# Performance work log

Hardware: AMD Instinct MI355X
Metric: run time of the kernel (lower is better)

Reference implementation:

```python
import jax, jax.numpy as jnp
import numpy as np
import math
from math import factorial

EPS = 1e-8
N_ATOMS = 20000
K_NEI = 32
N_RBF = 12
RBF_GAMMA = 1.0
DIMS = [(3, 24), (24, 12), (12, 4)]
# (i, f, o) = (input angular order, filter order, output order), from Convolution.C
CG_PATHS = [(0,0,0),(0,1,1),(1,0,1),(1,1,0),(1,1,1),(1,1,2),(0,2,2),(1,2,1),(1,2,2),(2,2,0),(2,2,1),(2,2,2),(2,0,2),(2,1,1),(2,1,2)]


def _su2_cg(j1, m1, j2, m2, j3, m3):
    if m3 != m1 + m2:
        return 0.0
    f = factorial
    vmin = int(max(-j1 + j2 + m3, -j1 + m1, 0))
    vmax = int(min(j2 + j3 + m1, j3 - j1 + j2, j3 + m3))
    c = ((2 * j3 + 1) * f(j3 + j1 - j2) * f(j3 - j1 + j2) * f(j1 + j2 - j3)
         * f(j3 + m3) * f(j3 - m3)
         / (f(j1 + j2 + j3 + 1) * f(j1 - m1) * f(j1 + m1) * f(j2 - m2) * f(j2 + m2))) ** 0.5
    s = 0.0
    for v in range(vmin, vmax + 1):
        s += (-1) ** (v + j2 + m2) * f(j2 + j3 + m1 - v) * f(j1 - m1 + v) / (
            f(v) * f(j3 - j1 + j2 - v) * f(j3 + m3 - v) * f(j1 - j2 - m3 + v))
    return c * s


def _q(l):
    # change of basis real->complex spherical harmonics (e3nn convention)
    q = np.zeros((2 * l + 1, 2 * l + 1), dtype=complex)
    for m in range(-l, 0):
        q[l + m, l + abs(m)] = 1 / np.sqrt(2)
        q[l + m, l - abs(m)] = -1j / np.sqrt(2)
    q[l, l] = 1.0
    for m in range(1, l + 1):
        q[l + m, l + abs(m)] = (-1) ** m / np.sqrt(2)
        q[l + m, l - abs(m)] = 1j * (-1) ** m / np.sqrt(2)
    return (-1j) ** l * q


def _real_cg(i, f, o):
    C = np.zeros((2 * i + 1, 2 * f + 1, 2 * o + 1), dtype=complex)
    for a, m1 in enumerate(range(-i, i + 1)):
        for b, m2 in enumerate(range(-f, f + 1)):
            for c, m3 in enumerate(range(-o, o + 1)):
                C[a, b, c] = _su2_cg(i, m1, f, m2, o, m3)
    C = np.einsum('ij,kl,mn,ikn->jlm', _q(i), _q(f), np.conj(_q(o).T), C)
    return np.real(C).transpose(2, 0, 1).astype(np.float32)  # [2o+1, 2i+1, 2f+1]


CG = {(i, f, o): jnp.asarray(_real_cg(i, f, o)) for (i, f, o) in CG_PATHS}
RBF_MU = jnp.asarray(np.linspace(0.0, 8.0, N_RBF).astype(np.float32))


def _sh(vec):
    # real spherical harmonics as in class Y (l=1 is the raw vector, l=2 divided by r^2)
    x, y, z = vec[..., 0], vec[..., 1], vec[..., 2]
    r2 = jnp.maximum(x * x + y * y + z * z, EPS)
    y2 = jnp.stack([x * y / r2,
                    y * z / r2,
                    (-x * x - y * y + 2.0 * z * z) / (2.0 * math.sqrt(3.0) * r2),
                    z * x / r2,
                    (x * x - y * y) / (2.0 * r2)], axis=-1)
    return {0: jnp.ones(vec.shape[:-1] + (1,), vec.dtype), 1: vec, 2: y2}


def _ssp(x):  # eta: shifted softplus (SchNet-style scalar nonlinearity)
    return jax.nn.softplus(x) - math.log(2.0)


def _self_interaction(V, w, b):
    O = {k: jnp.einsum('ncm,dc->ndm', Vk, w) for k, Vk in V.items()}
    O[0] = O[0] + b[None, :, None]  # bias only on angular order 0
    return O


def _model(V, nei_idx, Ys, rbf, siA_w, siA_b, rw1, rb1, rw2, rb2, siB_w, siB_b, nl_b):
    V = _self_interaction(V, siA_w, siA_b)
    N, C = nei_idx.shape[0], rw2.shape[1]
    O = {l: jnp.zeros((N, C, 2 * l + 1), rbf.dtype) for l in range(3)}
    for p, (i, f, o) in enumerate(CG_PATHS):
        # per-path radial MLP: 12 -> 12 (relu) -> C
        h = jax.nn.relu(jnp.einsum('nkb,hb->nkh', rbf, rw1[p]) + rb1[p])
        r = jnp.einsum('nkh,ch->nkc', h, rw2[p]) + rb2[p]              # [N,K,C]
        Vg = V[i][nei_idx]                                              # [N,K,C,2i+1]
        cif = jnp.einsum('nkc,nkf,nkci->ncif', r, Ys[f], Vg)            # sum over neighbors
        O[o] = O[o] + jnp.einsum('oif,ncif->nco', CG[(i, f, o)], cif)
    # Norm: per-atom L2 norm over (channel, m)
    V = {k: Vk / jnp.sqrt(jnp.maximum(jnp.sum(Vk * Vk, axis=(1, 2), keepdims=True), EPS))
         for k, Vk in O.items()}
    V = _self_interaction(V, siB_w, siB_b)
    # NonLinearity (faithful to source: norm is taken over ALL atoms and m, per channel)
    out = {0: _ssp(V[0])}
    for k in (1, 2):
        temp = jnp.sqrt(jnp.einsum('acm,acm->c', V[k], V[k])) + nl_b[k - 1]
        out[k] = V[k] * temp[None, :, None]
    return out


def _forward(atom_types, nei_idx, nei_vec, layers, dense):
    N = atom_types.shape[0]
    dt = nei_vec.dtype
    V = {0: jax.nn.one_hot(atom_types, 3, dtype=dt)[:, :, None],
         1: jnp.zeros((N, 3, 3), dt),
         2: jnp.zeros((N, 3, 5), dt)}
    dist = jnp.sqrt(jnp.maximum(jnp.sum(nei_vec * nei_vec, axis=-1), EPS))   # [N,K]
    rbf = jnp.exp(-RBF_GAMMA * (dist[..., None] - RBF_MU) ** 2)              # [N,K,12]
    Ys = _sh(nei_vec)
    for lp in layers:
        V = _model(V, nei_idx, Ys, rbf, *lp)
    E = jnp.sum(V[0], axis=0)[:, 0]                                          # [4]
    dw1, db1, dw2, db2, dw3, db3 = dense
    E = jax.nn.elu(dw1 @ E + db1)
    E = dw2 @ E + db2
    E = dw3 @ E + db3
    return E  # [1]


def setup_inputs() -> dict:
    key = jax.random.key(0)
    ks = iter(jax.random.split(key, 64))
    inp = {}
    inp['atom_types'] = jax.random.randint(next(ks), (N_ATOMS,), 0, 3, dtype=jnp.int32)
    inp['nei_idx'] = jax.random.randint(next(ks), (N_ATOMS, K_NEI), 0, N_ATOMS, dtype=jnp.int32)
    inp['nei_vec'] = jax.random.normal(next(ks), (N_ATOMS, K_NEI, 3), jnp.float32) * 2.0
    for l, (din, dout) in enumerate(DIMS, start=1):
        inp[f'l{l}_siA_w'] = jax.random.normal(next(ks), (dout, din)) / np.sqrt(din)
        inp[f'l{l}_siA_b'] = jnp.zeros((dout,))
        inp[f'l{l}_rw1'] = jax.random.normal(next(ks), (15, N_RBF, N_RBF)) / np.sqrt(N_RBF)
        inp[f'l{l}_rb1'] = jnp.zeros((15, N_RBF))
        inp[f'l{l}_rw2'] = jax.random.normal(next(ks), (15, dout, N_RBF)) / np.sqrt(N_RBF)
        inp[f'l{l}_rb2'] = jnp.zeros((15, dout))
        inp[f'l{l}_siB_w'] = jax.random.normal(next(ks), (dout, dout)) / np.sqrt(dout)
        inp[f'l{l}_siB_b'] = jnp.zeros((dout,))
        inp[f'l{l}_nl_b'] = jnp.zeros((2, dout))
    inp['dense_w1'] = jax.random.normal(next(ks), (4, 4)) * 0.5
    inp['dense_b1'] = jnp.zeros((4,))
    inp['dense_w2'] = jax.random.normal(next(ks), (256, 4)) * 0.5
    inp['dense_b2'] = jnp.zeros((256,))
    inp['dense_w3'] = jax.random.normal(next(ks), (1, 256)) / 16.0
    inp['dense_b3'] = jnp.zeros((1,))
    return inp


def reference(atom_types, nei_idx, nei_vec,
              l1_siA_w, l1_siA_b, l1_rw1, l1_rb1, l1_rw2, l1_rb2, l1_siB_w, l1_siB_b, l1_nl_b,
              l2_siA_w, l2_siA_b, l2_rw1, l2_rb1, l2_rw2, l2_rb2, l2_siB_w, l2_siB_b, l2_nl_b,
              l3_siA_w, l3_siA_b, l3_rw1, l3_rb1, l3_rw2, l3_rb2, l3_siB_w, l3_siB_b, l3_nl_b,
              dense_w1, dense_b1, dense_w2, dense_b2, dense_w3, dense_b3):
    layers = [
        (l1_siA_w, l1_siA_b, l1_rw1, l1_rb1, l1_rw2, l1_rb2, l1_siB_w, l1_siB_b, l1_nl_b),
        (l2_siA_w, l2_siA_b, l2_rw1, l2_rb1, l2_rw2, l2_rb2, l2_siB_w, l2_siB_b, l2_nl_b),
        (l3_siA_w, l3_siA_b, l3_rw1, l3_rb1, l3_rw2, l3_rb2, l3_siB_w, l3_siB_b, l3_nl_b),
    ]
    dense = (dense_w1, dense_b1, dense_w2, dense_b2, dense_w3, dense_b3)
    return _forward(atom_types, nei_idx, nei_vec, layers, dense)
```

## Files before the change

kernel.cpp:

```cpp
#include <hip/hip_runtime.h>
#include <math.h>

typedef long long i64;

#define EPSF 1e-8f

constexpr int NPATH = 15;
constexpr int PI_[NPATH] = {0,0,1,1,1,1,0,1,1,2,2,2,2,2,2};
constexpr int PF_[NPATH] = {0,1,0,1,1,1,2,2,2,2,2,2,0,1,1};
constexpr int PO_[NPATH] = {0,1,1,0,1,2,2,1,2,0,1,2,2,1,2};
constexpr int ISZ[NPATH] = {1,1,3,3,3,3,1,3,3,5,5,5,5,5,5};
constexpr int FSZ[NPATH] = {1,3,1,3,3,3,5,5,5,5,5,5,1,3,3};
constexpr int OSZ[NPATH] = {1,3,3,1,3,5,5,3,5,1,3,5,5,3,5};
constexpr int IBASE[NPATH] = {0,0,1,1,1,1,0,1,1,4,4,4,4,4,4};
constexpr int FBASE[NPATH] = {0,1,0,1,1,1,4,4,4,4,4,4,0,1,1};
constexpr int OBASE[NPATH] = {0,1,1,0,1,4,4,1,4,0,1,4,4,1,4};
constexpr int CGOFF[NPATH+1] = {0,1,10,19,28,55,100,125,170,245,270,345,470,495,540,615};
constexpr int GPOFF[NPATH+1] = {0,4,8,20,24,36,52,60,72,88,96,112,140,168,184,212};
constexpr int CGTOT = 615;
constexpr int GPTOT = 212;

__device__ double dfact(int n){ double r=1.0; for(int i=2;i<=n;++i) r*=(double)i; return r; }

__device__ double su2cg(int j1,int m1,int j2,int m2,int j3,int m3){
  if (m1+m2 != m3) return 0.0;
  int vmin = max(max(-j1+j2+m3, -j1+m1), 0);
  int vmax = min(min(j2+j3+m1, j3-j1+j2), j3+m3);
  if (vmax < vmin) return 0.0;
  double c = sqrt((double)(2*j3+1) * dfact(j3+j1-j2)*dfact(j3-j1+j2)*dfact(j1+j2-j3)
                  * dfact(j3+m3)*dfact(j3-m3)
                  / (dfact(j1+j2+j3+1)*dfact(j1-m1)*dfact(j1+m1)*dfact(j2-m2)*dfact(j2+m2)));
  double s = 0.0;
  for (int v=vmin; v<=vmax; ++v){
    double t = dfact(j2+j3+m1-v)*dfact(j1-m1+v)
             / (dfact(v)*dfact(j3-j1+j2-v)*dfact(j3+m3-v)*dfact(j1-j2-m3+v));
    s += ((v+j2+m2)&1) ? -t : t;
  }
  return c*s;
}

__device__ void qmat_lds(int l, double* qr, double* qi){
  for (int e=0;e<25;e++){ qr[e]=0.0; qi[e]=0.0; }
  const double s2 = 0.70710678118654752440;
  for (int m=-l; m<0; ++m){
    qr[(l+m)*5 + (l-m)] = s2;
    qi[(l+m)*5 + (l+m)] = -s2;
  }
  qr[l*5+l] = 1.0;
  for (int m=1; m<=l; ++m){
    double sg = (m&1)? -1.0 : 1.0;
    qr[(l+m)*5 + (l+m)] = sg*s2;
    qi[(l+m)*5 + (l-m)] = sg*s2;
  }
  if (l==1){
    for (int e=0;e<25;e++){ double r=qr[e], m=qi[e]; qr[e]=m; qi[e]=-r; }
  } else if (l==2){
    for (int e=0;e<25;e++){ qr[e]=-qr[e]; qi[e]=-qi[e]; }
  }
}

__global__ void cg_init_kernel(float* __restrict__ cg){
  int p = blockIdx.x;
  int li = PI_[p], lf = PF_[p], lo = PO_[p];
  int isz = 2*li+1, fsz = 2*lf+1, osz = 2*lo+1;
  __shared__ double sC[125];
  __shared__ double qir[25],qii[25],qfr[25],qfi[25],qor[25],qoi[25];
  if (threadIdx.x==0){
    qmat_lds(li,qir,qii); qmat_lds(lf,qfr,qfi); qmat_lds(lo,qor,qoi);
  }
  int tot = isz*fsz*osz;
  for (int e=threadIdx.x; e<tot; e+=blockDim.x){
    int a = e/(fsz*osz); int r = e%(fsz*osz); int b = r/osz; int n = r%osz;
    sC[e] = su2cg(li, a-li, lf, b-lf, lo, n-lo);
  }
  __syncthreads();
  for (int e=threadIdx.x; e<tot; e+=blockDim.x){
    int mo = e/(isz*fsz); int r = e%(isz*fsz); int ji = r/fsz; int lff = r%fsz;
    double acc = 0.0;
    for (int a=0;a<isz;a++) for(int b=0;b<fsz;b++) for(int n=0;n<osz;n++){
      double s = sC[(a*fsz+b)*osz+n];
      if (s==0.0) continue;
      double r1=qir[a*5+ji],  m1=qii[a*5+ji];
      double r2=qfr[b*5+lff], m2=qfi[b*5+lff];
      double r3=qor[n*5+mo],  m3=-qoi[n*5+mo];
      double rr = r1*r2 - m1*m2;
      double mm = r1*m2 + m1*r2;
      acc += (rr*r3 - mm*m3)*s;
    }
    cg[CGOFF[p] + (mo*isz+ji)*fsz + lff] = (float)acc;
  }
}

__device__ __forceinline__ float sspf(float x){
  float sp = (x > 20.f) ? x : log1pf(__expf(x));
  return sp - 0.69314718055994531f;
}

__global__ void siA1_kernel(const int* __restrict__ types, const float* __restrict__ w,
                            const float* __restrict__ b, float* __restrict__ Vp, int N){
  int idx = blockIdx.x*blockDim.x + threadIdx.x;
  if (idx >= N*24) return;
  int n = idx/24, d = idx%24;
  float v = w[d*3 + types[n]] + b[d];
  float* row = Vp + (i64)idx*12;
  row[0] = v;
  #pragma unroll
  for (int m=1;m<12;m++) row[m]=0.f;
}


template<int A, int P>
__device__ __forceinline__ void gphase(int t, const float* __restrict__ sY,
                                       const float* __restrict__ sCG, float* __restrict__ sG){
  if constexpr (P < NPATH){
    constexpr int gsz = OSZ[P]*ISZ[P];
    for (int e=t; e<gsz*A; e+=192){
      int a = e % A, rel = e / A;
      const float* cr = &sCG[CGOFF[P] + rel*FSZ[P]];
      const float* Yr = &sY[a*12 + FBASE[P]];
      float v = 0.f;
      #pragma unroll
      for (int f=0; f<FSZ[P]; ++f) v += cr[f]*Yr[f];
      sG[a*GPTOT + GPOFF[P] + rel] = v;
    }
    gphase<A,P+1>(t,sY,sCG,sG);
  }
}

template<int P, int V>
__device__ __forceinline__ void gstream(const float* __restrict__ sG_a,
                                        const float* vgr, float* acc){
  constexpr int gsz = OSZ[P]*ISZ[P];
  if constexpr (4*V < gsz){
    float4 g = *reinterpret_cast<const float4*>(&sG_a[GPOFF[P] + 4*V]);
    constexpr int e0 = 4*V;
    acc[OBASE[P] + (e0  )/ISZ[P]] += g.x * vgr[(e0  )%ISZ[P]];
    if constexpr (e0+1 < gsz) acc[OBASE[P] + (e0+1)/ISZ[P]] += g.y * vgr[(e0+1)%ISZ[P]];
    if constexpr (e0+2 < gsz) acc[OBASE[P] + (e0+2)/ISZ[P]] += g.z * vgr[(e0+2)%ISZ[P]];
    if constexpr (e0+3 < gsz) acc[OBASE[P] + (e0+3)/ISZ[P]] += g.w * vgr[(e0+3)%ISZ[P]];
    gstream<P,V+1>(sG_a,vgr,acc);
  }
}

template<int C, int P, int PEND>
__device__ __forceinline__ void ipath(const float* __restrict__ sw2c, const float* __restrict__ sb2,
                                      int c, const float* __restrict__ sh_a,
                                      const float* __restrict__ sG_a,
                                      const float* vg, float* acc){
  if constexpr (P < PEND){
    constexpr int NR2 = 15*C;
    float4 w0 = *reinterpret_cast<const float4*>(&sw2c[(0*NR2 + P*C + c)*4]);
    float4 w1 = *reinterpret_cast<const float4*>(&sw2c[(1*NR2 + P*C + c)*4]);
    float4 w2v= *reinterpret_cast<const float4*>(&sw2c[(2*NR2 + P*C + c)*4]);
    const float* h = &sh_a[P*12];
    float4 h0 = *reinterpret_cast<const float4*>(h);
    float4 h1 = *reinterpret_cast<const float4*>(h+4);
    float4 h2 = *reinterpret_cast<const float4*>(h+8);
    float rr = sb2[P*C+c]
      + w0.x*h0.x + w0.y*h0.y + w0.z*h0.z + w0.w*h0.w
      + w1.x*h1.x + w1.y*h1.y + w1.z*h1.z + w1.w*h1.w
      + w2v.x*h2.x + w2v.y*h2.y + w2v.z*h2.z + w2v.w*h2.w;
    float vgr[5];
    #pragma unroll
    for (int i=0; i<ISZ[P]; ++i) vgr[i] = rr * vg[IBASE[P]+i];
    gstream<P,0>(sG_a, vgr, acc);
    ipath<C,P+1,PEND>(sw2c,sb2,c,sh_a,sG_a,vg,acc);
  }
}

template<int C, int A, int PG>
__global__ __launch_bounds__(192) void conv_kernel(
    const float* __restrict__ Vp, const int* __restrict__ nei_idx, const float* __restrict__ nei_vec,
    const float* __restrict__ gw1, const float* __restrict__ gb1,
    const float* __restrict__ gw2, const float* __restrict__ gb2,
    const float* __restrict__ cg, float* __restrict__ O, int N)
{
  constexpr int T = 192;
  constexpr int GRP = A*C;
  static_assert(PG*GRP == T, "bad geometry");
  constexpr int NR2 = 15*C;
  __shared__ float sw1c[2160];
  __shared__ float sb1[180];
  __shared__ float sw2c[NR2*12];
  __shared__ float sb2[NR2];
  __shared__ float sCG[CGTOT];
  __shared__ float srbf[A*12];
  __shared__ float sY[A*12];
  __shared__ float sh[A*180];
  __shared__ float sG[A*GPTOT];

  const int t = threadIdx.x;
  const i64 atom0 = (i64)blockIdx.x * A;

  for (int e=t; e<2160; e+=T){
    int row = e/12, j = e - row*12;
    sw1c[((j>>2)*180 + row)*4 + (j&3)] = gw1[e];
  }
  for (int e=t; e<180;   e+=T) sb1[e]=gb1[e];
  for (int e=t; e<NR2*12; e+=T){
    int row = e/12, j = e - row*12;
    sw2c[((j>>2)*NR2 + row)*4 + (j&3)] = gw2[e];
  }
  for (int e=t; e<NR2;   e+=T) sb2[e]=gb2[e];
  for (int e=t; e<CGTOT; e+=T) sCG[e]=cg[e];

  auto stage = [&](int kn){
    if (t < A*12){
      int aa = t/12, j = t - aa*12;
      i64 at = atom0 + aa; if (at >= (i64)N) at = N-1;
      const float* vv = &nei_vec[(at*32 + kn)*3];
      float x=vv[0], y=vv[1], z=vv[2];
      float d = sqrtf(fmaxf(x*x+y*y+z*z, EPSF));
      float dd = d - 0.72727272727272727f*(float)j;
      srbf[t] = __expf(-dd*dd);
    }
    if (t < A){
      i64 at = atom0 + t; if (at >= (i64)N) at = N-1;
      const float* vv = &nei_vec[(at*32 + kn)*3];
      float x=vv[0], y=vv[1], z=vv[2];
      float r2 = fmaxf(x*x+y*y+z*z, EPSF);
      float inv = 1.f/r2;
      float* Ye = &sY[t*12];
      Ye[0]=1.f; Ye[1]=x; Ye[2]=y; Ye[3]=z;
      Ye[4]=x*y*inv; Ye[5]=y*z*inv;
      Ye[6]=(2.f*z*z - x*x - y*y)*(0.28867513459481287f*inv);
      Ye[7]=z*x*inv; Ye[8]=(x*x - y*y)*(0.5f*inv);
    }
  };

  stage(0);
  __syncthreads();

  const int pg  = (PG==1) ? 0 : (t/GRP);
  const int rem = (PG==1) ? t : (t%GRP);
  const int a = rem / C;
  const int c = rem % C;

  float acc[9];
  #pragma unroll
  for (int m=0;m<9;++m) acc[m]=0.f;

  for (int k=0; k<32; ++k){
    if (t < 180){
      float4 a0 = *reinterpret_cast<const float4*>(&sw1c[t*4]);
      float4 a1 = *reinterpret_cast<const float4*>(&sw1c[(180+t)*4]);
      float4 a2 = *reinterpret_cast<const float4*>(&sw1c[(360+t)*4]);
      float bb = sb1[t];
      for (int aa=0; aa<A; ++aa){
        const float* rb = &srbf[aa*12];
        float4 r0 = *reinterpret_cast<const float4*>(rb);
        float4 r1 = *reinterpret_cast<const float4*>(rb+4);
        float4 r2 = *reinterpret_cast<const float4*>(rb+8);
        float v = bb
          + a0.x*r0.x + a0.y*r0.y + a0.z*r0.z + a0.w*r0.w
          + a1.x*r1.x + a1.y*r1.y + a1.z*r1.z + a1.w*r1.w
          + a2.x*r2.x + a2.y*r2.y + a2.z*r2.z + a2.w*r2.w;
        sh[aa*180 + t] = fmaxf(v, 0.f);
      }
    }
    gphase<A,0>(t, sY, sCG, sG);
    __syncthreads();
    if (k+1 < 32) stage(k+1);
    {
      i64 at = atom0 + a; if (at >= (i64)N) at = N-1;
      int nei = nei_idx[at*32 + k];
      const float* vr = Vp + ((i64)nei*C + c)*12;
      float vg[9];
      float4 v0 = *reinterpret_cast<const float4*>(vr);
      float4 v1 = *reinterpret_cast<const float4*>(vr+4);
      vg[0]=v0.x; vg[1]=v0.y; vg[2]=v0.z; vg[3]=v0.w;
      vg[4]=v1.x; vg[5]=v1.y; vg[6]=v1.z; vg[7]=v1.w;
      vg[8]=vr[8];
      if constexpr (PG==1){
        ipath<C,0,NPATH>(sw2c,sb2,c,&sh[a*180],&sG[a*GPTOT],vg,acc);
      } else if constexpr (PG==2){
        if (pg==0) ipath<C,0,10>(sw2c,sb2,c,&sh[a*180],&sG[a*GPTOT],vg,acc);
        else       ipath<C,10,NPATH>(sw2c,sb2,c,&sh[a*180],&sG[a*GPTOT],vg,acc);
      } else {
        if      (pg==0) ipath<C,0,6>(sw2c,sb2,c,&sh[a*180],&sG[a*GPTOT],vg,acc);
        else if (pg==1) ipath<C,6,11>(sw2c,sb2,c,&sh[a*180],&sG[a*GPTOT],vg,acc);
        else            ipath<C,11,NPATH>(sw2c,sb2,c,&sh[a*180],&sG[a*GPTOT],vg,acc);
      }
    }
    __syncthreads();
  }

  i64 at = atom0 + a;
  if constexpr (PG==1){
    if (at < (i64)N){
      float* orow = O + (at*C + c)*12;
      *reinterpret_cast<float4*>(orow)   = make_float4(acc[0],acc[1],acc[2],acc[3]);
      *reinterpret_cast<float4*>(orow+4) = make_float4(acc[4],acc[5],acc[6],acc[7]);
      orow[8] = acc[8];
    }
  } else {
    if (pg > 0){
      float* red = &sh[((pg-1)*GRP + rem)*9];
      #pragma unroll
      for (int m=0;m<9;++m) red[m]=acc[m];
    }
    __syncthreads();
    if (pg==0 && at < (i64)N){
      #pragma unroll
      for (int g=1; g<PG; ++g){
        const float* red = &sh[((g-1)*GRP + rem)*9];
        #pragma unroll
        for (int m=0;m<9;++m) acc[m] += red[m];
      }
      float* orow = O + (at*C + c)*12;
      *reinterpret_cast<float4*>(orow)   = make_float4(acc[0],acc[1],acc[2],acc[3]);
      *reinterpret_cast<float4*>(orow+4) = make_float4(acc[4],acc[5],acc[6],acc[7]);
      orow[8] = acc[8];
    }
  }
}

template<int C>
__global__ __launch_bounds__(64) void normsiB_kernel(
    const float* __restrict__ O, const float* __restrict__ w, const float* __restrict__ b,
    float* __restrict__ Vb, float* __restrict__ gsum, int N)
{
  __shared__ float sW[C*C];
  __shared__ float sO[C*9];
  __shared__ float sg[2*C];
  const int t = threadIdx.x;
  for (int e=t; e<C*C; e+=64) sW[e]=w[e];
  for (int e=t; e<2*C; e+=64) sg[e]=0.f;
  __syncthreads();
  const int iters = (N + gridDim.x - 1)/gridDim.x;
  for (int it=0; it<iters; ++it){
    i64 at = (i64)blockIdx.x + (i64)it*gridDim.x;
    float p0=0.f,p1=0.f,p2=0.f;
    if (at<(i64)N){
      for (int e=t; e<C*9; e+=64){
        int cc=e/9, m=e-cc*9;
        float v = O[((i64)at*C+cc)*12+m];
        sO[e]=v;
        float vv=v*v;
        if (m==0) p0+=vv; else if (m<4) p1+=vv; else p2+=vv;
      }
    }
    #pragma unroll
    for (int off=1; off<64; off<<=1){
      p0 += __shfl_xor(p0, off);
      p1 += __shfl_xor(p1, off);
      p2 += __shfl_xor(p2, off);
    }
    float i0 = 1.f/sqrtf(fmaxf(p0, EPSF));
    float i1 = 1.f/sqrtf(fmaxf(p1, EPSF));
    float i2 = 1.f/sqrtf(fmaxf(p2, EPSF));
    __syncthreads();
    if (at<(i64)N){
      for (int e=t; e<C*9; e+=64){
        int d=e/9, m=e-d*9;
        float inv = (m==0)? i0 : (m<4)? i1 : i2;
        const float* wr = &sW[d*C];
        float s=0.f;
        #pragma unroll
        for (int cc=0; cc<C; ++cc) s += wr[cc]*sO[cc*9+m];
        float outv = s*inv + ((m==0)? b[d] : 0.f);
        Vb[((i64)at*C+d)*12+m]=outv;
        if (m>=1) atomicAdd(&sg[(m<4?0:1)*C + d], outv*outv);
      }
    }
    __syncthreads();
  }
  for (int e=t; e<2*C; e+=64) atomicAdd(&gsum[e], sg[e]);
}

template<int Ci, int Co>
__global__ __launch_bounds__(64) void siaNL_kernel(
    const float* __restrict__ Vb, const float* __restrict__ gsum, const float* __restrict__ nlb,
    const float* __restrict__ w, const float* __restrict__ b, float* __restrict__ Vp, int N)
{
  __shared__ float sW[Co*Ci];
  __shared__ float sIn[Ci*9];
  __shared__ float sT[2*Ci];
  const int t=threadIdx.x;
  for (int e=t; e<Co*Ci; e+=64) sW[e]=w[e];
  for (int e=t; e<2*Ci;  e+=64) sT[e] = sqrtf(gsum[e]) + nlb[e];
  __syncthreads();
  const int iters = (N + gridDim.x - 1)/gridDim.x;
  for (int it=0; it<iters; ++it){
    i64 at = (i64)blockIdx.x + (i64)it*gridDim.x;
    if (at<(i64)N){
      for (int e=t; e<Ci*9; e+=64){
        int cc=e/9, m=e-cc*9;
        float v = Vb[((i64)at*Ci+cc)*12+m];
        float x = (m==0)? sspf(v) : (m<4)? v*sT[cc] : v*sT[Ci+cc];
        sIn[e]=x;
      }
    }
    __syncthreads();
    if (at<(i64)N){
      for (int e=t; e<Co*9; e+=64){
        int d=e/9, m=e-d*9;
        const float* wr=&sW[d*Ci];
        float s = (m==0)? b[d] : 0.f;
        #pragma unroll
        for (int cc=0;cc<Ci;++cc) s += wr[cc]*sIn[cc*9+m];
        Vp[((i64)at*Co+d)*12+m]=s;
      }
    }
    __syncthreads();
  }
}

__global__ void final_reduce_kernel(const float* __restrict__ Vb, float* __restrict__ Eacc, int N){
  __shared__ float sE[4];
  const int t=threadIdx.x;
  if (t<4) sE[t]=0.f;
  __syncthreads();
  float a0=0.f,a1=0.f,a2=0.f,a3=0.f;
  for (i64 at = (i64)blockIdx.x*blockDim.x + t; at < (i64)N; at += (i64)gridDim.x*blockDim.x){
    const float* row = Vb + at*4*12;
    a0 += sspf(row[0]);  a1 += sspf(row[12]);
    a2 += sspf(row[24]); a3 += sspf(row[36]);
  }
  atomicAdd(&sE[0],a0); atomicAdd(&sE[1],a1);
  atomicAdd(&sE[2],a2); atomicAdd(&sE[3],a3);
  __syncthreads();
  if (t<4) atomicAdd(&Eacc[t], sE[t]);
}

__global__ void final_dense_kernel(const float* __restrict__ Eacc,
    const float* __restrict__ w1,const float* __restrict__ b1,
    const float* __restrict__ w2,const float* __restrict__ b2,
    const float* __restrict__ w3,const float* __restrict__ b3,
    float* __restrict__ out)
{
  __shared__ float sE1[4];
  __shared__ float sH[256];
  const int t=threadIdx.x;
  if (t<4){
    float v=b1[t];
    #pragma unroll
    for (int j=0;j<4;j++) v += w1[t*4+j]*Eacc[j];
    sE1[t] = (v>0.f)? v : expm1f(v);
  }
  __syncthreads();
  {
    float v=b2[t];
    #pragma unroll
    for (int j=0;j<4;j++) v += w2[t*4+j]*sE1[j];
    sH[t]=v;
  }
  __syncthreads();
  if (t==0){
    float s=b3[0];
    for (int j=0;j<256;j++) s += w3[j]*sH[j];
    out[0]=s;
  }
}

extern "C" void kernel_launch(void* const* d_in, const int* in_sizes, int n_in,
                              void* d_out, int out_size, void* d_ws, size_t ws_size,
                              hipStream_t stream)
{
  const int* atom_types = (const int*)d_in[0];
  const int* nei_idx    = (const int*)d_in[1];
  const float* nei_vec  = (const float*)d_in[2];
  const float* in_f[36];
  for (int i=0;i<36 && i<n_in;i++) in_f[i] = (const float*)d_in[i];
  const int N = in_sizes[0];

  const i64 bsz = (i64)N*24*12;
  const size_t needed = 8192 + (size_t)3*bsz*4;
  if (ws_size < needed) return;

  char* ws = (char*)d_ws;
  float* cg   = (float*)ws;
  float* accs = (float*)(ws + 4096);
  float* gs1 = accs; float* gs2 = accs+48; float* gs3 = accs+72; float* Eacc = accs+80;
  float* bufA = (float*)(ws + 8192);
  float* bufB = bufA + bsz;
  float* bufC = bufB + bsz;

  #define LP(l, j) in_f[3 + 9*(l) + (j)]
  hipMemsetAsync(accs, 0, 512, stream);
  cg_init_kernel<<<15, 64, 0, stream>>>(cg);

  siA1_kernel<<<(N*24+255)/256, 256, 0, stream>>>(atom_types, LP(0,0), LP(0,1), bufB, N);
  conv_kernel<24,8,1><<<(N+7)/8, 192, 0, stream>>>(bufB, nei_idx, nei_vec,
      LP(0,2),LP(0,3),LP(0,4),LP(0,5), cg, bufC, N);
  normsiB_kernel<24><<<2048,64,0,stream>>>(bufC, LP(0,6), LP(0,7), bufA, gs1, N);
  siaNL_kernel<24,12><<<2048,64,0,stream>>>(bufA, gs1, LP(0,8), LP(1,0), LP(1,1), bufB, N);
  conv_kernel<12,16,1><<<(N+15)/16, 192, 0, stream>>>(bufB, nei_idx, nei_vec,
      LP(1,2),LP(1,3),LP(1,4),LP(1,5), cg, bufC, N);
  normsiB_kernel<12><<<2048,64,0,stream>>>(bufC, LP(1,6), LP(1,7), bufA, gs2, N);
  siaNL_kernel<12,4><<<2048,64,0,stream>>>(bufA, gs2, LP(1,8), LP(2,0), LP(2,1), bufB, N);
  conv_kernel<4,16,3><<<(N+15)/16, 192, 0, stream>>>(bufB, nei_idx, nei_vec,
      LP(2,2),LP(2,3),LP(2,4),LP(2,5), cg, bufC, N);
  normsiB_kernel<4><<<2048,64,0,stream>>>(bufC, LP(2,6), LP(2,7), bufA, gs3, N);
  final_reduce_kernel<<<128,256,0,stream>>>(bufA, Eacc, N);
  final_dense_kernel<<<1,256,0,stream>>>(Eacc, in_f[30],in_f[31],in_f[32],in_f[33],in_f[34],in_f[35],
                                         (float*)d_out);
  #undef LP
}
```

Measured before the change: 2.202 ms.

## Add multi-channel-per-thread conv kernel for the first two layers

Introduces a convM kernel where each thread handles several output channels (CPT), so the shared Clebsch-Gordan product terms and radial-filter hidden activations are reused across channels held in registers. More atoms are processed per block (24 or 32 instead of 8 or 16), and the RBF, spherical harmonics and per-atom G computation move into per-thread registers. Layers 1 and 2 use the new kernel, while layer 3 keeps the old one, renamed convB. The cost is higher register pressure and larger shared memory per block, which may reduce occupancy.

```diff
diff --git a/kernel.cpp b/kernel.cpp
--- a/kernel.cpp
+++ b/kernel.cpp
@@ -106,6 +106,174 @@
   row[0] = v;
   #pragma unroll
   for (int m=1;m<12;m++) row[m]=0.f;
+}
+
+
+template<int CS, int P>
+__device__ __forceinline__ void gphaseM(int a, int cs, const float* __restrict__ Yreg,
+                                        const float* __restrict__ sCG, float* __restrict__ sG){
+  if constexpr (P < NPATH){
+    constexpr int gsz = OSZ[P]*ISZ[P];
+    for (int rel=cs; rel<gsz; rel+=CS){
+      const float* cr = &sCG[CGOFF[P] + rel*FSZ[P]];
+      float v = 0.f;
+      #pragma unroll
+      for (int f=0; f<FSZ[P]; ++f) v += cr[f]*Yreg[FBASE[P]+f];
+      sG[a*GPTOT + GPOFF[P] + rel] = v;
+    }
+    gphaseM<CS,P+1>(a,cs,Yreg,sCG,sG);
+  }
+}
+
+template<int P, int V, int CPT>
+__device__ __forceinline__ void gstreamM(const float* __restrict__ sG_a,
+                                         const float* vgr, float* acc){
+  constexpr int gsz = OSZ[P]*ISZ[P];
+  if constexpr (4*V < gsz){
+    float4 g = *reinterpret_cast<const float4*>(&sG_a[GPOFF[P] + 4*V]);
+    constexpr int e0 = 4*V;
+    #pragma unroll
+    for (int ch=0; ch<CPT; ++ch){
+      acc[ch*9 + OBASE[P] + (e0  )/ISZ[P]] += g.x * vgr[ch*5 + (e0  )%ISZ[P]];
+      if constexpr (e0+1 < gsz) acc[ch*9 + OBASE[P] + (e0+1)/ISZ[P]] += g.y * vgr[ch*5 + (e0+1)%ISZ[P]];
+      if constexpr (e0+2 < gsz) acc[ch*9 + OBASE[P] + (e0+2)/ISZ[P]] += g.z * vgr[ch*5 + (e0+2)%ISZ[P]];
+      if constexpr (e0+3 < gsz) acc[ch*9 + OBASE[P] + (e0+3)/ISZ[P]] += g.w * vgr[ch*5 + (e0+3)%ISZ[P]];
+    }
+    gstreamM<P,V+1,CPT>(sG_a,vgr,acc);
+  }
+}
+
+template<int C, int CPT, int CS, int P, int PEND>
+__device__ __forceinline__ void ipathM(const float* __restrict__ sw2c, const float* __restrict__ sb2,
+                                       int cs, const float* __restrict__ sh_a,
+                                       const float* __restrict__ sG_a,
+                                       const float* vg, float* acc){
+  if constexpr (P < PEND){
+    constexpr int NR2 = 15*C;
+    const float* h = &sh_a[P*12];
+    float4 h0 = *reinterpret_cast<const float4*>(h);
+    float4 h1 = *reinterpret_cast<const float4*>(h+4);
+    float4 h2 = *reinterpret_cast<const float4*>(h+8);
+    float rr[CPT];
+    #pragma unroll
+    for (int ch=0; ch<CPT; ++ch){
+      int row = P*C + cs + ch*CS;
+      float4 w0 = *reinterpret_cast<const float4*>(&sw2c[(0*NR2 + row)*4]);
+      float4 w1 = *reinterpret_cast<const float4*>(&sw2c[(1*NR2 + row)*4]);
+      float4 w2v= *reinterpret_cast<const float4*>(&sw2c[(2*NR2 + row)*4]);
+      rr[ch] = sb2[row]
+        + w0.x*h0.x + w0.y*h0.y + w0.z*h0.z + w0.w*h0.w
+        + w1.x*h1.x + w1.y*h1.y + w1.z*h1.z + w1.w*h1.w
+        + w2v.x*h2.x + w2v.y*h2.y + w2v.z*h2.z + w2v.w*h2.w;
+    }
+    float vgr[CPT*5];
+    #pragma unroll
+    for (int ch=0; ch<CPT; ++ch){
+      #pragma unroll
+      for (int i=0; i<ISZ[P]; ++i) vgr[ch*5+i] = rr[ch] * vg[ch*9 + IBASE[P]+i];
+    }
+    gstreamM<P,0,CPT>(sG_a, vgr, acc);
+    ipathM<C,CPT,CS,P+1,PEND>(sw2c,sb2,cs,sh_a,sG_a,vg,acc);
+  }
+}
+
+template<int C, int CPT, int A>
+__global__ __launch_bounds__(A*(C/CPT)) void convM_kernel(
+    const float* __restrict__ Vp, const int* __restrict__ nei_idx, const float* __restrict__ nei_vec,
+    const float* __restrict__ gw1, const float* __restrict__ gb1,
+    const float* __restrict__ gw2, const float* __restrict__ gb2,
+    const float* __restrict__ cg, float* __restrict__ O, int N)
+{
+  constexpr int CS = C/CPT;
+  constexpr int T = A*CS;
+  static_assert(C % CPT == 0, "bad CPT");
+  constexpr int NR2 = 15*C;
+  __shared__ float sw1c[2160];
+  __shared__ float sb1[180];
+  __shared__ float sw2c[NR2*12];
+  __shared__ float sb2[NR2];
+  __shared__ float sCG[CGTOT];
+  __shared__ float sh[A*180];
+  __shared__ float sG[A*GPTOT];
+
+  const int t = threadIdx.x;
+  const i64 atom0 = (i64)blockIdx.x * A;
+  const int a  = t / CS;
+  const int cs = t % CS;
+
+  for (int e=t; e<2160; e+=T){
+    int row = e/12, j = e - row*12;
+    sw1c[((j>>2)*180 + row)*4 + (j&3)] = gw1[e];
+  }
+  for (int e=t; e<180; e+=T) sb1[e]=gb1[e];
+  for (int e=t; e<NR2*12; e+=T){
+    int row = e/12, j = e - row*12;
+    sw2c[((j>>2)*NR2 + row)*4 + (j&3)] = gw2[e];
+  }
+  for (int e=t; e<NR2;   e+=T) sb2[e]=gb2[e];
+  for (int e=t; e<CGTOT; e+=T) sCG[e]=cg[e];
+  __syncthreads();
+
+  float acc[CPT*9];
+  #pragma unroll
+  for (int e=0; e<CPT*9; ++e) acc[e]=0.f;
+
+  i64 atR = atom0 + a; if (atR >= (i64)N) atR = N-1;
+
+  for (int k=0; k<32; ++k){
+    {
+      const float* vv = &nei_vec[(atR*32 + k)*3];
+      float x=vv[0], y=vv[1], z=vv[2];
+      float r2 = fmaxf(x*x+y*y+z*z, EPSF);
+      float d = sqrtf(r2), inv = 1.f/r2;
+      float rb[12];
+      #pragma unroll
+      for (int j=0;j<12;++j){ float dd = d - 0.72727272727272727f*(float)j; rb[j] = __expf(-dd*dd); }
+      float Yreg[9];
+      Yreg[0]=1.f; Yreg[1]=x; Yreg[2]=y; Yreg[3]=z;
+      Yreg[4]=x*y*inv; Yreg[5]=y*z*inv;
+      Yreg[6]=(2.f*z*z - x*x - y*y)*(0.28867513459481287f*inv);
+      Yreg[7]=z*x*inv; Yreg[8]=(x*x - y*y)*(0.5f*inv);
+      for (int row=cs; row<180; row+=CS){
+        float4 w0 = *reinterpret_cast<const float4*>(&sw1c[row*4]);
+        float4 w1 = *reinterpret_cast<const float4*>(&sw1c[(180+row)*4]);
+        float4 w2v= *reinterpret_cast<const float4*>(&sw1c[(360+row)*4]);
+        float v = sb1[row]
+          + w0.x*rb[0] + w0.y*rb[1] + w0.z*rb[2]  + w0.w*rb[3]
+          + w1.x*rb[4] + w1.y*rb[5] + w1.z*rb[6]  + w1.w*rb[7]
+          + w2v.x*rb[8] + w2v.y*rb[9] + w2v.z*rb[10] + w2v.w*rb[11];
+        sh[a*180 + row] = fmaxf(v, 0.f);
+      }
+      gphaseM<CS,0>(a, cs, Yreg, sCG, sG);
+    }
+    __syncthreads();
+    {
+      int nei = nei_idx[atR*32 + k];
+      float vg[CPT*9];
+      #pragma unroll
+      for (int ch=0; ch<CPT; ++ch){
+        const float* vr = &Vp[((i64)nei*C + cs + ch*CS)*12];
+        float4 v0 = *reinterpret_cast<const float4*>(vr);
+        float4 v1 = *reinterpret_cast<const float4*>(vr+4);
+        vg[ch*9+0]=v0.x; vg[ch*9+1]=v0.y; vg[ch*9+2]=v0.z; vg[ch*9+3]=v0.w;
+        vg[ch*9+4]=v1.x; vg[ch*9+5]=v1.y; vg[ch*9+6]=v1.z; vg[ch*9+7]=v1.w;
+        vg[ch*9+8]=vr[8];
+      }
+      ipathM<C,CPT,CS,0,NPATH>(sw2c, sb2, cs, &sh[a*180], &sG[a*GPTOT], vg, acc);
+    }
+    __syncthreads();
+  }
+
+  i64 at = atom0 + a;
+  if (at < (i64)N){
+    #pragma unroll
+    for (int ch=0; ch<CPT; ++ch){
+      float* orow = O + (at*C + cs + ch*CS)*12;
+      *reinterpret_cast<float4*>(orow)   = make_float4(acc[ch*9+0],acc[ch*9+1],acc[ch*9+2],acc[ch*9+3]);
+      *reinterpret_cast<float4*>(orow+4) = make_float4(acc[ch*9+4],acc[ch*9+5],acc[ch*9+6],acc[ch*9+7]);
+      orow[8] = acc[ch*9+8];
+    }
+  }
 }
 
 
@@ -169,7 +337,7 @@
 }
 
 template<int C, int A, int PG>
-__global__ __launch_bounds__(192) void conv_kernel(
+__global__ __launch_bounds__(192) void convB_kernel(
     const float* __restrict__ Vp, const int* __restrict__ nei_idx, const float* __restrict__ nei_vec,
     const float* __restrict__ gw1, const float* __restrict__ gb1,
     const float* __restrict__ gw2, const float* __restrict__ gb2,
@@ -481,15 +649,15 @@
   cg_init_kernel<<<15, 64, 0, stream>>>(cg);
 
   siA1_kernel<<<(N*24+255)/256, 256, 0, stream>>>(atom_types, LP(0,0), LP(0,1), bufB, N);
-  conv_kernel<24,8,1><<<(N+7)/8, 192, 0, stream>>>(bufB, nei_idx, nei_vec,
+  convM_kernel<24,3,24><<<(N+23)/24, 192, 0, stream>>>(bufB, nei_idx, nei_vec,
       LP(0,2),LP(0,3),LP(0,4),LP(0,5), cg, bufC, N);
   normsiB_kernel<24><<<2048,64,0,stream>>>(bufC, LP(0,6), LP(0,7), bufA, gs1, N);
   siaNL_kernel<24,12><<<2048,64,0,stream>>>(bufA, gs1, LP(0,8), LP(1,0), LP(1,1), bufB, N);
-  conv_kernel<12,16,1><<<(N+15)/16, 192, 0, stream>>>(bufB, nei_idx, nei_vec,
+  convM_kernel<12,2,32><<<(N+31)/32, 192, 0, stream>>>(bufB, nei_idx, nei_vec,
       LP(1,2),LP(1,3),LP(1,4),LP(1,5), cg, bufC, N);
   normsiB_kernel<12><<<2048,64,0,stream>>>(bufC, LP(1,6), LP(1,7), bufA, gs2, N);
   siaNL_kernel<12,4><<<2048,64,0,stream>>>(bufA, gs2, LP(1,8), LP(2,0), LP(2,1), bufB, N);
-  conv_kernel<4,16,3><<<(N+15)/16, 192, 0, stream>>>(bufB, nei_idx, nei_vec,
+  convB_kernel<4,16,3><<<(N+15)/16, 192, 0, stream>>>(bufB, nei_idx, nei_vec,
       LP(2,2),LP(2,3),LP(2,4),LP(2,5), cg, bufC, N);
   normsiB_kernel<4><<<2048,64,0,stream>>>(bufC, LP(2,6), LP(2,7), bufA, gs3, N);
   final_reduce_kernel<<<128,256,0,stream>>>(bufA, Eacc, N);
```

Result: slower. 2.821 ms (+28.1%).

## Split conv paths across two thread groups with 384-thread blocks for layers 1-2

Applied to the files above, without the earlier changes.

The first two convolution layers now run 384-thread blocks where two thread groups each handle a subset of the 15 CG paths (split at path 9), with partial accumulators reduced through shared memory. The radial MLP first layer is spread across the extra threads via a replication factor, and a dedicated reduction buffer is added when the scratch array is too small. This aims to raise per-block parallelism and shorten each thread's serial path loop, at the cost of an extra reduction, a larger block and possibly lower occupancy.

```diff
diff --git a/kernel.cpp b/kernel.cpp
--- a/kernel.cpp
+++ b/kernel.cpp
@@ -109,12 +109,12 @@
 }
 
 
-template<int A, int P>
+template<int A, int T, int P>
 __device__ __forceinline__ void gphase(int t, const float* __restrict__ sY,
                                        const float* __restrict__ sCG, float* __restrict__ sG){
   if constexpr (P < NPATH){
     constexpr int gsz = OSZ[P]*ISZ[P];
-    for (int e=t; e<gsz*A; e+=192){
+    for (int e=t; e<gsz*A; e+=T){
       int a = e % A, rel = e / A;
       const float* cr = &sCG[CGOFF[P] + rel*FSZ[P]];
       const float* Yr = &sY[a*12 + FBASE[P]];
@@ -123,7 +123,7 @@
       for (int f=0; f<FSZ[P]; ++f) v += cr[f]*Yr[f];
       sG[a*GPTOT + GPOFF[P] + rel] = v;
     }
-    gphase<A,P+1>(t,sY,sCG,sG);
+    gphase<A,T,P+1>(t,sY,sCG,sG);
   }
 }
 
@@ -168,17 +168,22 @@
   }
 }
 
-template<int C, int A, int PG>
-__global__ __launch_bounds__(192) void conv_kernel(
+template<int C, int A, int PG, int T, int PSPLIT>
+__global__ __launch_bounds__(T) void conv_kernel(
     const float* __restrict__ Vp, const int* __restrict__ nei_idx, const float* __restrict__ nei_vec,
     const float* __restrict__ gw1, const float* __restrict__ gb1,
     const float* __restrict__ gw2, const float* __restrict__ gb2,
     const float* __restrict__ cg, float* __restrict__ O, int N)
 {
-  constexpr int T = 192;
   constexpr int GRP = A*C;
   static_assert(PG*GRP == T, "bad geometry");
+  static_assert(GRP % 64 == 0, "path group not wave-aligned");
+  constexpr int REP = T/192;
+  static_assert(A % REP == 0, "bad REP");
   constexpr int NR2 = 15*C;
+  constexpr bool RED_IN_SH = ((PG-1)*GRP*9 <= A*180);
+  constexpr int REDSZ = RED_IN_SH ? 1 : (PG-1)*GRP*9;
+
   __shared__ float sw1c[2160];
   __shared__ float sb1[180];
   __shared__ float sw2c[NR2*12];
@@ -188,6 +193,7 @@
   __shared__ float sY[A*12];
   __shared__ float sh[A*180];
   __shared__ float sG[A*GPTOT];
+  __shared__ float sRed[REDSZ];
 
   const int t = threadIdx.x;
   const i64 atom0 = (i64)blockIdx.x * A;
@@ -241,12 +247,16 @@
   for (int m=0;m<9;++m) acc[m]=0.f;
 
   for (int k=0; k<32; ++k){
-    if (t < 180){
-      float4 a0 = *reinterpret_cast<const float4*>(&sw1c[t*4]);
-      float4 a1 = *reinterpret_cast<const float4*>(&sw1c[(180+t)*4]);
-      float4 a2 = *reinterpret_cast<const float4*>(&sw1c[(360+t)*4]);
-      float bb = sb1[t];
-      for (int aa=0; aa<A; ++aa){
+    if (t < 180*REP){
+      const int row = (REP==1) ? t : (t % 180);
+      const int sl  = (REP==1) ? 0 : (t / 180);
+      float4 a0 = *reinterpret_cast<const float4*>(&sw1c[row*4]);
+      float4 a1 = *reinterpret_cast<const float4*>(&sw1c[(180+row)*4]);
+      float4 a2 = *reinterpret_cast<const float4*>(&sw1c[(360+row)*4]);
+      float bb = sb1[row];
+      #pragma unroll
+      for (int q=0; q<A/REP; ++q){
+        const int aa = sl*(A/REP) + q;
         const float* rb = &srbf[aa*12];
         float4 r0 = *reinterpret_cast<const float4*>(rb);
         float4 r1 = *reinterpret_cast<const float4*>(rb+4);
@@ -255,10 +265,10 @@
           + a0.x*r0.x + a0.y*r0.y + a0.z*r0.z + a0.w*r0.w
           + a1.x*r1.x + a1.y*r1.y + a1.z*r1.z + a1.w*r1.w
           + a2.x*r2.x + a2.y*r2.y + a2.z*r2.z + a2.w*r2.w;
-        sh[aa*180 + t] = fmaxf(v, 0.f);
-      }
-    }
-    gphase<A,0>(t, sY, sCG, sG);
+        sh[aa*180 + row] = fmaxf(v, 0.f);
+      }
+    }
+    gphase<A,T,0>(t, sY, sCG, sG);
     __syncthreads();
     if (k+1 < 32) stage(k+1);
     {
@@ -274,8 +284,8 @@
       if constexpr (PG==1){
         ipath<C,0,NPATH>(sw2c,sb2,c,&sh[a*180],&sG[a*GPTOT],vg,acc);
       } else if constexpr (PG==2){
-        if (pg==0) ipath<C,0,10>(sw2c,sb2,c,&sh[a*180],&sG[a*GPTOT],vg,acc);
-        else       ipath<C,10,NPATH>(sw2c,sb2,c,&sh[a*180],&sG[a*GPTOT],vg,acc);
+        if (pg==0) ipath<C,0,PSPLIT>(sw2c,sb2,c,&sh[a*180],&sG[a*GPTOT],vg,acc);
+        else       ipath<C,PSPLIT,NPATH>(sw2c,sb2,c,&sh[a*180],&sG[a*GPTOT],vg,acc);
       } else {
         if      (pg==0) ipath<C,0,6>(sw2c,sb2,c,&sh[a*180],&sG[a*GPTOT],vg,acc);
         else if (pg==1) ipath<C,6,11>(sw2c,sb2,c,&sh[a*180],&sG[a*GPTOT],vg,acc);
@@ -294,8 +304,9 @@
       orow[8] = acc[8];
     }
   } else {
+    float* redbuf = RED_IN_SH ? sh : sRed;
     if (pg > 0){
-      float* red = &sh[((pg-1)*GRP + rem)*9];
+      float* red = &redbuf[((pg-1)*GRP + rem)*9];
       #pragma unroll
       for (int m=0;m<9;++m) red[m]=acc[m];
     }
@@ -303,7 +314,7 @@
     if (pg==0 && at < (i64)N){
       #pragma unroll
       for (int g=1; g<PG; ++g){
-        const float* red = &sh[((g-1)*GRP + rem)*9];
+        const float* red = &redbuf[((g-1)*GRP + rem)*9];
         #pragma unroll
         for (int m=0;m<9;++m) acc[m] += red[m];
       }
@@ -481,15 +492,15 @@
   cg_init_kernel<<<15, 64, 0, stream>>>(cg);
 
   siA1_kernel<<<(N*24+255)/256, 256, 0, stream>>>(atom_types, LP(0,0), LP(0,1), bufB, N);
-  conv_kernel<24,8,1><<<(N+7)/8, 192, 0, stream>>>(bufB, nei_idx, nei_vec,
+  conv_kernel<24,8,2,384,9><<<(N+7)/8, 384, 0, stream>>>(bufB, nei_idx, nei_vec,
       LP(0,2),LP(0,3),LP(0,4),LP(0,5), cg, bufC, N);
   normsiB_kernel<24><<<2048,64,0,stream>>>(bufC, LP(0,6), LP(0,7), bufA, gs1, N);
   siaNL_kernel<24,12><<<2048,64,0,stream>>>(bufA, gs1, LP(0,8), LP(1,0), LP(1,1), bufB, N);
-  conv_kernel<12,16,1><<<(N+15)/16, 192, 0, stream>>>(bufB, nei_idx, nei_vec,
+  conv_kernel<12,16,2,384,9><<<(N+15)/16, 384, 0, stream>>>(bufB, nei_idx, nei_vec,
       LP(1,2),LP(1,3),LP(1,4),LP(1,5), cg, bufC, N);
   normsiB_kernel<12><<<2048,64,0,stream>>>(bufC, LP(1,6), LP(1,7), bufA, gs2, N);
   siaNL_kernel<12,4><<<2048,64,0,stream>>>(bufA, gs2, LP(1,8), LP(2,0), LP(2,1), bufB, N);
-  conv_kernel<4,16,3><<<(N+15)/16, 192, 0, stream>>>(bufB, nei_idx, nei_vec,
+  conv_kernel<4,16,3,192,0><<<(N+15)/16, 192, 0, stream>>>(bufB, nei_idx, nei_vec,
       LP(2,2),LP(2,3),LP(2,4),LP(2,5), cg, bufC, N);
   normsiB_kernel<4><<<2048,64,0,stream>>>(bufC, LP(2,6), LP(2,7), bufA, gs3, N);
   final_reduce_kernel<<<128,256,0,stream>>>(bufA, Eacc, N);
```

Result: slower. 2.537 ms (+15.2%).
